# Kernel tuning notes

Measured on AMD Instinct MI355X. Metric: run time of the kernel, lower is better.

## Reference

```python
import jax, jax.numpy as jnp
import numpy as np

N = 10000
E = 160000
D_IN = 512
D_HID = 512


def gcn_conv(x, W, b, src, dst, norm, num_nodes):
    # x: [N, Fin] -> h: [N, Fout]; PyG GCNConv: linear transform, then
    # symmetric-normalized aggregation over edges with self-loops.
    h = x @ W + b  # [N, Fout]
    msgs = h[src] * norm[:, None]  # [E', Fout]
    return jax.ops.segment_sum(msgs, dst, num_segments=num_nodes)


def _norm_with_self_loops(edge_index, num_nodes):
    loop = jnp.arange(num_nodes, dtype=edge_index.dtype)
    src = jnp.concatenate([edge_index[0], loop])
    dst = jnp.concatenate([edge_index[1], loop])
    deg = jax.ops.segment_sum(jnp.ones_like(dst, dtype=jnp.float32), dst,
                              num_segments=num_nodes)
    dis = jnp.where(deg > 0, jax.lax.rsqrt(jnp.maximum(deg, 1.0)), 0.0)
    norm = dis[src] * dis[dst]
    return src, dst, norm


def setup_inputs() -> dict:
    key = jax.random.key(0)
    ks = jax.random.split(key, 8)
    x = jax.random.normal(ks[0], (N, D_IN), dtype=jnp.float32)
    edge_index = jax.random.randint(ks[1], (2, E), 0, N, dtype=jnp.int64)
    s1 = 1.0 / np.sqrt(D_IN)
    s2 = 1.0 / np.sqrt(D_HID)
    W1 = jax.random.uniform(ks[2], (D_IN, D_HID), jnp.float32, -s1, s1)
    b1 = jnp.zeros((D_HID,), jnp.float32)
    W2 = jax.random.uniform(ks[3], (D_HID, D_IN), jnp.float32, -s2, s2)
    b2 = jnp.zeros((D_IN,), jnp.float32)
    Wp1 = jax.random.uniform(ks[4], (D_HID, D_HID), jnp.float32, -s2, s2)
    bp1 = jnp.zeros((D_HID,), jnp.float32)
    Wp2 = jax.random.uniform(ks[5], (D_HID, D_HID), jnp.float32, -s2, s2)
    bp2 = jnp.zeros((D_HID,), jnp.float32)
    return {"x": x, "edge_index": edge_index, "W1": W1, "b1": b1,
            "W2": W2, "b2": b2, "Wp1": Wp1, "bp1": bp1,
            "Wp2": Wp2, "bp2": bp2}


def reference(x, edge_index, W1, b1, W2, b2, Wp1, bp1, Wp2, bp2):
    num_nodes = x.shape[0]
    src, dst, norm = _norm_with_self_loops(edge_index, num_nodes)
    z = gcn_conv(x, W1, b1, src, dst, norm, num_nodes)        # [N, hidden]
    h = jax.nn.relu(z)
    out = gcn_conv(h, W2, b2, src, dst, norm, num_nodes)      # [N, in]
    proj = jax.nn.relu(z @ Wp1 + bp1) @ Wp2 + bp2             # [N, hidden]
    return (out, z, proj)
```

## Files before the change

### kernel.cpp

```cpp
#include <hip/hip_runtime.h>
#include <stddef.h>

#define N_NODES 10000
#define N_EDGES 160000
#define DIM     512
#define RBT     158
#define RB128   79
#define GBLKS   (RB128 * 4)
#define EBLKS   625
#define PAKBLKS (RBT * 16)
#define MAXDEG  64

typedef short bf16x8 __attribute__((ext_vector_type(8)));
typedef float f32x4  __attribute__((ext_vector_type(4)));

__device__ inline unsigned short bf16_rne(float f) {
    unsigned u = __builtin_bit_cast(unsigned, f);
    u += 0x7FFF + ((u >> 16) & 1);
    return (unsigned short)(u >> 16);
}
__device__ inline float bf16_to_f32(unsigned short h) {
    unsigned u = ((unsigned)h) << 16;
    return __builtin_bit_cast(float, u);
}

__device__ inline void gld_lds16(const void* g, void* lds) {
    __builtin_amdgcn_global_load_lds(
        (const __attribute__((address_space(1))) void*)g,
        (__attribute__((address_space(3))) void*)lds, 16, 0, 0);
}

__device__ __forceinline__ bf16x8 relu_pk(bf16x8 v) {
    bf16x8 r;
#pragma unroll
    for (int i = 0; i < 8; ++i) r[i] = (v[i] < (short)0) ? (short)0 : v[i];
    return r;
}


__global__ __launch_bounds__(256) void prep_kernel(
    const float* __restrict__ W1, const float* __restrict__ W2,
    const float* __restrict__ Wp1, const float* __restrict__ Wp2,
    short* __restrict__ T1, short* __restrict__ T2,
    short* __restrict__ Tp1, short* __restrict__ Tp2,
    const float* __restrict__ X, short* __restrict__ APKx,
    const int* __restrict__ ei, int* __restrict__ deg)
{
    const int bid = blockIdx.x;
    if (bid < 512) {
        const int wsel = bid >> 7;
        const float* W = (wsel == 0) ? W1 : (wsel == 1) ? W2 : (wsel == 2) ? Wp1 : Wp2;
        short* WT      = (wsel == 0) ? T1 : (wsel == 1) ? T2 : (wsel == 2) ? Tp1 : Tp2;
        int id = (bid & 127) * 256 + threadIdx.x;
        int n  = id & 511;
        int kc = id >> 9;
        int colblk = n >> 6, col = n & 63;
        int kt = kc >> 2, kq = kc & 3;
        short hi[8];
#pragma unroll
        for (int j = 0; j < 8; ++j)
            hi[j] = (short)bf16_rne(W[(size_t)(kc * 8 + j) * 512 + n]);
        size_t base = (size_t)(colblk * 16 + kt) * 2048 + col * 32 + ((kq ^ ((col >> 1) & 3)) << 3);
        *(int4*)(WT + base) = *(const int4*)hi;
    } else if (bid < 512 + PAKBLKS) {
        const int pb = bid - 512;
        const int kt = pb & 15;
        const int rb = pb >> 4;
        const int t  = threadIdx.x;
        const int r  = t >> 2;
        const int kq = t & 3;
        const int row = rb * 64 + r;
        float v[8] = {};
        if (row < N_NODES) {
            float4 a = *(const float4*)(X + (size_t)row * 512 + kt * 32 + kq * 8);
            float4 b = *(const float4*)(X + (size_t)row * 512 + kt * 32 + kq * 8 + 4);
            v[0]=a.x; v[1]=a.y; v[2]=a.z; v[3]=a.w; v[4]=b.x; v[5]=b.y; v[6]=b.z; v[7]=b.w;
        }
        short hi[8];
#pragma unroll
        for (int j = 0; j < 8; ++j) hi[j] = (short)bf16_rne(v[j]);
        size_t base = (size_t)(rb * 16 + kt) * 2048 + r * 32 + ((kq ^ ((r >> 1) & 3)) << 3);
        *(int4*)(APKx + base) = *(const int4*)hi;
    } else {
        int e = (bid - 512 - PAKBLKS) * 256 + threadIdx.x;
        if (e < N_EDGES) atomicAdd(&deg[ei[N_EDGES + e]], 1);
    }
}


__global__ __launch_bounds__(256) void deg2dis_kernel(const int* __restrict__ deg,
                                                      float* __restrict__ dis,
                                                      int* __restrict__ cursor, int n) {
    int i = blockIdx.x * 256 + threadIdx.x;
    if (i < n) {
        dis[i] = rsqrtf((float)(deg[i] + 1));
        cursor[i] = 0;
    }
}


__device__ __forceinline__ void map_block(int bid, int& rb, int& cb) {
    const int q = GBLKS / 8;
    const int r = GBLKS % 8;
    int xcd = bid & 7;
    int idx = bid >> 3;
    int L = (xcd < r ? xcd * (q + 1) : r * (q + 1) + (xcd - r) * q) + idx;
    rb = L >> 2;
    cb = L & 3;
}

template<bool RELU_A>
__device__ __forceinline__ void gemm128_core(
    const short* __restrict__ Apk, const short* __restrict__ Wpk,
    int bid, f32x4 (&acc)[4][4],
    short (*As)[4096], short (*Bs)[4096],
    int& rb, int& cb, int& wr, int& wc)
{
    map_block(bid, rb, cb);
    const int tid = threadIdx.x;
    const int w = tid >> 6;
    wr = w >> 1;
    wc = w & 1;
    const int lane = tid & 63;
    const int l15 = lane & 15, kg = lane >> 4;
    const int kso = ((kg ^ ((l15 >> 1) & 3)) << 3);
    const int wofs = w * 1024;

    const char* At0 = (const char*)(Apk + (size_t)(rb * 2)     * 16 * 2048);
    const char* At1 = (const char*)(Apk + (size_t)(rb * 2 + 1) * 16 * 2048);
    const char* Bt0 = (const char*)(Wpk + (size_t)(cb * 2)     * 16 * 2048);
    const char* Bt1 = (const char*)(Wpk + (size_t)(cb * 2 + 1) * 16 * 2048);

#pragma unroll
    for (int i = 0; i < 4; ++i)
#pragma unroll
        for (int j = 0; j < 4; ++j) acc[i][j] = (f32x4){0.f, 0.f, 0.f, 0.f};

    auto stage = [&](int buf, int kt) {
        const int go = kt * 4096 + tid * 16;
        char* ad = (char*)&As[buf][0];
        char* bd = (char*)&Bs[buf][0];
        gld_lds16(At0 + go, ad + wofs);
        gld_lds16(At1 + go, ad + 4096 + wofs);
        gld_lds16(Bt0 + go, bd + wofs);
        gld_lds16(Bt1 + go, bd + 4096 + wofs);
    };

    stage(0, 0);
    stage(1, 1);

#pragma unroll
    for (int kt = 0; kt < 16; ++kt) {
        const int buf = kt % 3;
        if (kt < 15) {
            asm volatile("s_waitcnt vmcnt(4)" ::: "memory");
        } else {
            asm volatile("s_waitcnt vmcnt(0)" ::: "memory");
        }
        __builtin_amdgcn_s_barrier();
        __builtin_amdgcn_sched_barrier(0);
        if (kt < 14) stage((kt + 2) % 3, kt + 2);

        const short* as = &As[buf][wr * 2048];
        const short* bs = &Bs[buf][wc * 2048];
        bf16x8 af[4], bf[4];
#pragma unroll
        for (int m = 0; m < 4; ++m) {
            af[m] = *(const bf16x8*)&as[(m * 16 + l15) * 32 + kso];
            if (RELU_A) af[m] = relu_pk(af[m]);
        }
#pragma unroll
        for (int n = 0; n < 4; ++n)
            bf[n] = *(const bf16x8*)&bs[(n * 16 + l15) * 32 + kso];
#pragma unroll
        for (int m = 0; m < 4; ++m)
#pragma unroll
            for (int n = 0; n < 4; ++n)
                acc[m][n] = __builtin_amdgcn_mfma_f32_16x16x32_bf16(af[m], bf[n], acc[m][n], 0, 0, 0);
    }
}


template<bool RELU_OUT>
__device__ __forceinline__ void epi128_f32(f32x4 (&acc)[4][4], const float* bias,
                                           float* C, int rb, int cb, int wr, int wc) {
    const int lane = threadIdx.x & 63;
    const int l15 = lane & 15, kg = lane >> 4;
#pragma unroll
    for (int n = 0; n < 4; ++n) {
        int c = cb * 128 + wc * 64 + n * 16 + l15;
        float bv = bias[c];
#pragma unroll
        for (int m = 0; m < 4; ++m) {
            int r0 = rb * 128 + wr * 64 + m * 16 + kg * 4;
#pragma unroll
            for (int j = 0; j < 4; ++j) {
                int row = r0 + j;
                if (row < N_NODES) {
                    float v = acc[m][n][j] + bv;
                    if (RELU_OUT) v = fmaxf(v, 0.f);
                    C[(size_t)row * 512 + c] = v;
                }
            }
        }
    }
}

__device__ __forceinline__ void epi128_bf16(f32x4 (&acc)[4][4], const float* bias,
                                            unsigned short* C, int rb, int cb, int wr, int wc) {
    const int lane = threadIdx.x & 63;
    const int l15 = lane & 15, kg = lane >> 4;
#pragma unroll
    for (int n = 0; n < 4; ++n) {
        int c = cb * 128 + wc * 64 + n * 16 + l15;
        float bv = bias[c];
#pragma unroll
        for (int m = 0; m < 4; ++m) {
            int r0 = rb * 128 + wr * 64 + m * 16 + kg * 4;
#pragma unroll
            for (int j = 0; j < 4; ++j) {
                int row = r0 + j;
                if (row < N_NODES)
                    C[(size_t)row * 512 + c] = bf16_rne(acc[m][n][j] + bv);
            }
        }
    }
}

__device__ __forceinline__ void epi128_pack(f32x4 (&acc)[4][4], const float* bias,
                                            short* Cpk, int rb, int cb, int wr, int wc) {
    const int lane = threadIdx.x & 63;
    const int l15 = lane & 15, kg = lane >> 4;
#pragma unroll
    for (int n = 0; n < 4; ++n) {
        int c = cb * 128 + wc * 64 + n * 16 + l15;
        int kt_n = c >> 5, kk = c & 31, kgn = kk >> 3, kj = kk & 7;
        float bv = bias[c];
#pragma unroll
        for (int m = 0; m < 4; ++m) {
#pragma unroll
            for (int j = 0; j < 4; ++j) {
                int grow = rb * 128 + wr * 64 + m * 16 + kg * 4 + j;
                float v = (grow < N_NODES) ? fmaxf(acc[m][n][j] + bv, 0.f) : 0.f;
                int rt = grow >> 6, rl = grow & 63;
                size_t dst = (size_t)(rt * 16 + kt_n) * 2048 + rl * 32
                           + ((kgn ^ ((rl >> 1) & 3)) << 3) + kj;
                Cpk[dst] = (short)bf16_rne(v);
            }
        }
    }
}


__global__ __launch_bounds__(256, 3) void gemm1_scatter_kernel(
    const short* __restrict__ APKx, const short* __restrict__ WT1,
    const float* __restrict__ b1, unsigned short* __restrict__ Hb,
    const int* __restrict__ ei, const float* __restrict__ dis,
    int* __restrict__ cursor,
    int* __restrict__ csr_src, float* __restrict__ csr_norm)
{
    __shared__ short As[3][4096];
    __shared__ short Bs[3][4096];
    const int bid = blockIdx.x;
    if (bid >= GBLKS) {
        int e = (bid - GBLKS) * 256 + threadIdx.x;
        if (e < N_EDGES) {
            int s = ei[e];
            int d = ei[N_EDGES + e];
            int slot = d * MAXDEG + atomicAdd(&cursor[d], 1);
            csr_src[slot]  = s;
            csr_norm[slot] = dis[s] * dis[d];
        }
        return;
    }
    f32x4 acc[4][4];
    int rb, cb, wr, wc;
    gemm128_core<false>(APKx, WT1, bid, acc, As, Bs, rb, cb, wr, wc);
    epi128_bf16(acc, b1, Hb, rb, cb, wr, wc);
}


__global__ __launch_bounds__(256) void agg1_pack_kernel(
    const unsigned short* __restrict__ Hb,
    const float* __restrict__ dis,
    const int* __restrict__ deg,
    const int* __restrict__ csr_src,
    const float* __restrict__ csr_norm,
    float* __restrict__ z,
    short* __restrict__ ZPKp)
{
    const int node = blockIdx.x * 2 + (threadIdx.x >> 7);
    const int q = threadIdx.x & 127;
    const int f0 = q * 4;
    const int kt = f0 >> 5, kq = (f0 >> 3) & 3, j = f0 & 7;
    const int rb = node >> 6, r = node & 63;
    const size_t dst = (size_t)(rb * 16 + kt) * 2048 + r * 32 + ((kq ^ ((r >> 1) & 3)) << 3) + j;

    if (node >= N_NODES) {
        *(ushort4*)(ZPKp + dst) = make_ushort4(0, 0, 0, 0);
        return;
    }

    const int base = node * MAXDEG;
    const int end  = base + deg[node];
    const float dn = dis[node];
    const float sw = dn * dn;

    ushort4 hv = *((const ushort4*)(Hb + (size_t)node * DIM) + q);
    float a0 = bf16_to_f32(hv.x) * sw;
    float a1 = bf16_to_f32(hv.y) * sw;
    float a2 = bf16_to_f32(hv.z) * sw;
    float a3 = bf16_to_f32(hv.w) * sw;

    int e = base;
    for (; e + 7 < end; e += 8) {
        int s[8]; float w[8]; ushort4 v[8];
#pragma unroll
        for (int i = 0; i < 8; ++i) { s[i] = csr_src[e + i]; w[i] = csr_norm[e + i]; }
#pragma unroll
        for (int i = 0; i < 8; ++i) v[i] = *((const ushort4*)(Hb + (size_t)s[i] * DIM) + q);
#pragma unroll
        for (int i = 0; i < 8; ++i) {
            a0 += bf16_to_f32(v[i].x) * w[i];
            a1 += bf16_to_f32(v[i].y) * w[i];
            a2 += bf16_to_f32(v[i].z) * w[i];
            a3 += bf16_to_f32(v[i].w) * w[i];
        }
    }
    for (; e < end; ++e) {
        int si = csr_src[e];
        float wi = csr_norm[e];
        ushort4 vi = *((const ushort4*)(Hb + (size_t)si * DIM) + q);
        a0 += bf16_to_f32(vi.x) * wi;
        a1 += bf16_to_f32(vi.y) * wi;
        a2 += bf16_to_f32(vi.z) * wi;
        a3 += bf16_to_f32(vi.w) * wi;
    }
    *((float4*)(z + (size_t)node * DIM) + q) = make_float4(a0, a1, a2, a3);
    *(ushort4*)(ZPKp + dst) = make_ushort4(bf16_rne(a0), bf16_rne(a1), bf16_rne(a2), bf16_rne(a3));
}


__global__ __launch_bounds__(256, 3) void gemm23_kernel(
    const short* __restrict__ ZPKp, const short* __restrict__ WT2,
    const float* __restrict__ b2, unsigned short* __restrict__ Hb,
    const short* __restrict__ WTp1,
    const float* __restrict__ bp1, short* __restrict__ APKp1)
{
    __shared__ short As[3][4096];
    __shared__ short Bs[3][4096];
    const int bid = blockIdx.x;
    f32x4 acc[4][4];
    int rb, cb, wr, wc;
    if (bid < GBLKS) {
        gemm128_core<true>(ZPKp, WT2, bid, acc, As, Bs, rb, cb, wr, wc);
        epi128_bf16(acc, b2, Hb, rb, cb, wr, wc);
    } else {
        gemm128_core<false>(ZPKp, WTp1, bid - GBLKS, acc, As, Bs, rb, cb, wr, wc);
        epi128_pack(acc, bp1, APKp1, rb, cb, wr, wc);
    }
}


__global__ __launch_bounds__(256) void agg2_kernel(
    const unsigned short* __restrict__ Hb, const float* __restrict__ dis,
    const int* __restrict__ deg, const int* __restrict__ csr_src,
    const float* __restrict__ csr_norm, float* __restrict__ out)
{
    const int node = blockIdx.x * 2 + (threadIdx.x >> 7);
    const int q = threadIdx.x & 127;

    const int base = node * MAXDEG;
    const int end  = base + deg[node];
    const float dn = dis[node];
    const float sw = dn * dn;

    ushort4 hv = *((const ushort4*)(Hb + (size_t)node * DIM) + q);
    float a0 = bf16_to_f32(hv.x) * sw;
    float a1 = bf16_to_f32(hv.y) * sw;
    float a2 = bf16_to_f32(hv.z) * sw;
    float a3 = bf16_to_f32(hv.w) * sw;

    int e = base;
    for (; e + 7 < end; e += 8) {
        int s[8]; float w[8]; ushort4 v[8];
#pragma unroll
        for (int i = 0; i < 8; ++i) { s[i] = csr_src[e + i]; w[i] = csr_norm[e + i]; }
#pragma unroll
        for (int i = 0; i < 8; ++i) v[i] = *((const ushort4*)(Hb + (size_t)s[i] * DIM) + q);
#pragma unroll
        for (int i = 0; i < 8; ++i) {
            a0 += bf16_to_f32(v[i].x) * w[i];
            a1 += bf16_to_f32(v[i].y) * w[i];
            a2 += bf16_to_f32(v[i].z) * w[i];
            a3 += bf16_to_f32(v[i].w) * w[i];
        }
    }
    for (; e < end; ++e) {
        int si = csr_src[e];
        float wi = csr_norm[e];
        ushort4 vi = *((const ushort4*)(Hb + (size_t)si * DIM) + q);
        a0 += bf16_to_f32(vi.x) * wi;
        a1 += bf16_to_f32(vi.y) * wi;
        a2 += bf16_to_f32(vi.z) * wi;
        a3 += bf16_to_f32(vi.w) * wi;
    }
    *((float4*)(out + (size_t)node * DIM) + q) = make_float4(a0, a1, a2, a3);
}


__global__ __launch_bounds__(256, 3) void gemm4_kernel(
    const short* __restrict__ APKp1, const short* __restrict__ WTp2,
    const float* __restrict__ bp2, float* __restrict__ proj)
{
    __shared__ short As[3][4096];
    __shared__ short Bs[3][4096];
    f32x4 acc[4][4];
    int rb, cb, wr, wc;
    gemm128_core<false>(APKp1, WTp2, blockIdx.x, acc, As, Bs, rb, cb, wr, wc);
    epi128_f32<false>(acc, bp2, proj, rb, cb, wr, wc);
}


extern "C" void kernel_launch(void* const* d_in, const int* in_sizes, int n_in,
                              void* d_out, int out_size, void* d_ws, size_t ws_size,
                              hipStream_t stream) {
    const float* x   = (const float*)d_in[0];
    const int*   ei  = (const int*)d_in[1];
    const float* W1  = (const float*)d_in[2];
    const float* b1  = (const float*)d_in[3];
    const float* W2  = (const float*)d_in[4];
    const float* b2  = (const float*)d_in[5];
    const float* Wp1 = (const float*)d_in[6];
    const float* bp1 = (const float*)d_in[7];
    const float* Wp2 = (const float*)d_in[8];
    const float* bp2 = (const float*)d_in[9];

    float* out  = (float*)d_out;
    float* z    = out + (size_t)N_NODES * DIM;
    float* proj = z   + (size_t)N_NODES * DIM;

    char* ws = (char*)d_ws;
    size_t off = 0;
    auto walloc = [&](size_t bytes) -> void* {
        void* p = ws + off;
        off = (off + bytes + 255) & ~(size_t)255;
        return p;
    };
    const size_t PK_SHORTS = (size_t)RBT * 16 * 2048;
    unsigned short* Hb = (unsigned short*)walloc((size_t)N_NODES * DIM * sizeof(unsigned short));
    short* APKx  = (short*)walloc(PK_SHORTS * sizeof(short));
    short* ZPKp  = (short*)walloc(PK_SHORTS * sizeof(short));
    short* APKp1 = (short*)walloc(PK_SHORTS * sizeof(short));
    short* WT1  = (short*)walloc((size_t)8 * 16 * 2048 * sizeof(short));
    short* WT2  = (short*)walloc((size_t)8 * 16 * 2048 * sizeof(short));
    short* WTp1 = (short*)walloc((size_t)8 * 16 * 2048 * sizeof(short));
    short* WTp2 = (short*)walloc((size_t)8 * 16 * 2048 * sizeof(short));
    int*   deg      = (int*)  walloc(N_NODES * sizeof(int));
    int*   cursor   = (int*)  walloc(N_NODES * sizeof(int));
    float* dis      = (float*)walloc(N_NODES * sizeof(float));
    int*   csr_src  = (int*)  walloc((size_t)N_NODES * MAXDEG * sizeof(int));
    float* csr_norm = (float*)walloc((size_t)N_NODES * MAXDEG * sizeof(float));

    const dim3 blk(256);

    hipMemsetAsync(deg, 0, N_NODES * sizeof(int), stream);
    prep_kernel<<<dim3(512 + PAKBLKS + EBLKS), blk, 0, stream>>>(
        W1, W2, Wp1, Wp2, WT1, WT2, WTp1, WTp2, x, APKx, ei, deg);
    deg2dis_kernel<<<dim3((N_NODES + 255) / 256), blk, 0, stream>>>(deg, dis, cursor, N_NODES);

    gemm1_scatter_kernel<<<dim3(GBLKS + EBLKS), blk, 0, stream>>>(
        APKx, WT1, b1, Hb, ei, dis, cursor, csr_src, csr_norm);
    agg1_pack_kernel<<<dim3(RB128 * 64), blk, 0, stream>>>(
        Hb, dis, deg, csr_src, csr_norm, z, ZPKp);
    gemm23_kernel<<<dim3(2 * GBLKS), blk, 0, stream>>>(
        ZPKp, WT2, b2, Hb, WTp1, bp1, APKp1);
    agg2_kernel<<<dim3(N_NODES / 2), blk, 0, stream>>>(
        Hb, dis, deg, csr_src, csr_norm, out);
    gemm4_kernel<<<dim3(GBLKS), blk, 0, stream>>>(APKp1, WTp2, bp2, proj);
}
```

Baseline: 146.7 us.

## Drop deg2dis kernel and split agg2 into feature panels

Removes the separate deg2dis kernel. Consumers now compute rsqrt(deg+1) inline, and one memset clears degree and cursor together, which saves a launch and a dependency step. The second aggregation is restructured into four feature panels of 128 columns, with 8 nodes per block and 32 lanes per node. This keeps the gathered Hb working set per panel smaller, for better L2 reuse. In exchange, each CSR index and weight is read four times and more blocks are launched.

```diff
diff --git a/kernel.cpp b/kernel.cpp
--- a/kernel.cpp
+++ b/kernel.cpp
@@ -10,6 +10,7 @@
 #define EBLKS   625
 #define PAKBLKS (RBT * 16)
 #define MAXDEG  64
+#define AGG2_NB 1250
 
 typedef short bf16x8 __attribute__((ext_vector_type(8)));
 typedef float f32x4  __attribute__((ext_vector_type(4)));
@@ -88,17 +89,6 @@
 }
 
 
-__global__ __launch_bounds__(256) void deg2dis_kernel(const int* __restrict__ deg,
-                                                      float* __restrict__ dis,
-                                                      int* __restrict__ cursor, int n) {
-    int i = blockIdx.x * 256 + threadIdx.x;
-    if (i < n) {
-        dis[i] = rsqrtf((float)(deg[i] + 1));
-        cursor[i] = 0;
-    }
-}
-
-
 __device__ __forceinline__ void map_block(int bid, int& rb, int& cb) {
     const int q = GBLKS / 8;
     const int r = GBLKS % 8;
@@ -255,7 +245,7 @@
 __global__ __launch_bounds__(256, 3) void gemm1_scatter_kernel(
     const short* __restrict__ APKx, const short* __restrict__ WT1,
     const float* __restrict__ b1, unsigned short* __restrict__ Hb,
-    const int* __restrict__ ei, const float* __restrict__ dis,
+    const int* __restrict__ ei, const int* __restrict__ deg,
     int* __restrict__ cursor,
     int* __restrict__ csr_src, float* __restrict__ csr_norm)
 {
@@ -269,7 +259,7 @@
             int d = ei[N_EDGES + e];
             int slot = d * MAXDEG + atomicAdd(&cursor[d], 1);
             csr_src[slot]  = s;
-            csr_norm[slot] = dis[s] * dis[d];
+            csr_norm[slot] = rsqrtf((float)(deg[s] + 1)) * rsqrtf((float)(deg[d] + 1));
         }
         return;
     }
@@ -282,7 +272,6 @@
 
 __global__ __launch_bounds__(256) void agg1_pack_kernel(
     const unsigned short* __restrict__ Hb,
-    const float* __restrict__ dis,
     const int* __restrict__ deg,
     const int* __restrict__ csr_src,
     const float* __restrict__ csr_norm,
@@ -303,7 +292,7 @@
 
     const int base = node * MAXDEG;
     const int end  = base + deg[node];
-    const float dn = dis[node];
+    const float dn = rsqrtf((float)(deg[node] + 1));
     const float sw = dn * dn;
 
     ushort4 hv = *((const ushort4*)(Hb + (size_t)node * DIM) + q);
@@ -362,20 +351,24 @@
 }
 
 
-__global__ __launch_bounds__(256) void agg2_kernel(
-    const unsigned short* __restrict__ Hb, const float* __restrict__ dis,
-    const int* __restrict__ deg, const int* __restrict__ csr_src,
-    const float* __restrict__ csr_norm, float* __restrict__ out)
-{
-    const int node = blockIdx.x * 2 + (threadIdx.x >> 7);
-    const int q = threadIdx.x & 127;
+__global__ __launch_bounds__(256) void agg2_panel_kernel(
+    const unsigned short* __restrict__ Hb,
+    const int* __restrict__ deg,
+    const int* __restrict__ csr_src,
+    const float* __restrict__ csr_norm,
+    float* __restrict__ out)
+{
+    const int panel = blockIdx.x / AGG2_NB;
+    const int nb    = blockIdx.x - panel * AGG2_NB;
+    const int node  = nb * 8 + (threadIdx.x >> 5);
+    const int fq    = panel * 32 + (threadIdx.x & 31);
 
     const int base = node * MAXDEG;
     const int end  = base + deg[node];
-    const float dn = dis[node];
+    const float dn = rsqrtf((float)(deg[node] + 1));
     const float sw = dn * dn;
 
-    ushort4 hv = *((const ushort4*)(Hb + (size_t)node * DIM) + q);
+    ushort4 hv = *((const ushort4*)(Hb + (size_t)node * DIM) + fq);
     float a0 = bf16_to_f32(hv.x) * sw;
     float a1 = bf16_to_f32(hv.y) * sw;
     float a2 = bf16_to_f32(hv.z) * sw;
@@ -387,7 +380,7 @@
 #pragma unroll
         for (int i = 0; i < 8; ++i) { s[i] = csr_src[e + i]; w[i] = csr_norm[e + i]; }
 #pragma unroll
-        for (int i = 0; i < 8; ++i) v[i] = *((const ushort4*)(Hb + (size_t)s[i] * DIM) + q);
+        for (int i = 0; i < 8; ++i) v[i] = *((const ushort4*)(Hb + (size_t)s[i] * DIM) + fq);
 #pragma unroll
         for (int i = 0; i < 8; ++i) {
             a0 += bf16_to_f32(v[i].x) * w[i];
@@ -399,13 +392,13 @@
     for (; e < end; ++e) {
         int si = csr_src[e];
         float wi = csr_norm[e];
-        ushort4 vi = *((const ushort4*)(Hb + (size_t)si * DIM) + q);
+        ushort4 vi = *((const ushort4*)(Hb + (size_t)si * DIM) + fq);
         a0 += bf16_to_f32(vi.x) * wi;
         a1 += bf16_to_f32(vi.y) * wi;
         a2 += bf16_to_f32(vi.z) * wi;
         a3 += bf16_to_f32(vi.w) * wi;
     }
-    *((float4*)(out + (size_t)node * DIM) + q) = make_float4(a0, a1, a2, a3);
+    *((float4*)(out + (size_t)node * DIM) + fq) = make_float4(a0, a1, a2, a3);
 }
 
 
@@ -456,26 +449,25 @@
     short* WT2  = (short*)walloc((size_t)8 * 16 * 2048 * sizeof(short));
     short* WTp1 = (short*)walloc((size_t)8 * 16 * 2048 * sizeof(short));
     short* WTp2 = (short*)walloc((size_t)8 * 16 * 2048 * sizeof(short));
-    int*   deg      = (int*)  walloc(N_NODES * sizeof(int));
-    int*   cursor   = (int*)  walloc(N_NODES * sizeof(int));
-    float* dis      = (float*)walloc(N_NODES * sizeof(float));
+    int*   degcur   = (int*)  walloc((size_t)2 * N_NODES * sizeof(int));
+    int*   deg      = degcur;
+    int*   cursor   = degcur + N_NODES;
     int*   csr_src  = (int*)  walloc((size_t)N_NODES * MAXDEG * sizeof(int));
     float* csr_norm = (float*)walloc((size_t)N_NODES * MAXDEG * sizeof(float));
 
     const dim3 blk(256);
 
-    hipMemsetAsync(deg, 0, N_NODES * sizeof(int), stream);
+    hipMemsetAsync(degcur, 0, (size_t)2 * N_NODES * sizeof(int), stream);
     prep_kernel<<<dim3(512 + PAKBLKS + EBLKS), blk, 0, stream>>>(
         W1, W2, Wp1, Wp2, WT1, WT2, WTp1, WTp2, x, APKx, ei, deg);
-    deg2dis_kernel<<<dim3((N_NODES + 255) / 256), blk, 0, stream>>>(deg, dis, cursor, N_NODES);
 
     gemm1_scatter_kernel<<<dim3(GBLKS + EBLKS), blk, 0, stream>>>(
-        APKx, WT1, b1, Hb, ei, dis, cursor, csr_src, csr_norm);
+        APKx, WT1, b1, Hb, ei, deg, cursor, csr_src, csr_norm);
     agg1_pack_kernel<<<dim3(RB128 * 64), blk, 0, stream>>>(
-        Hb, dis, deg, csr_src, csr_norm, z, ZPKp);
+        Hb, deg, csr_src, csr_norm, z, ZPKp);
     gemm23_kernel<<<dim3(2 * GBLKS), blk, 0, stream>>>(
         ZPKp, WT2, b2, Hb, WTp1, bp1, APKp1);
-    agg2_kernel<<<dim3(N_NODES / 2), blk, 0, stream>>>(
-        Hb, dis, deg, csr_src, csr_norm, out);
+    agg2_panel_kernel<<<dim3(4 * AGG2_NB), blk, 0, stream>>>(
+        Hb, deg, csr_src, csr_norm, out);
     gemm4_kernel<<<dim3(GBLKS), blk, 0, stream>>>(APKp1, WTp2, bp2, proj);
 }
```

After: 162.5 us. 1.11x slower.
